# Kernel tuning notes

Hardware: AMD Instinct MI355X
Metric: run time of the kernel (lower is better)

## Reference

```python
import jax, jax.numpy as jnp
import numpy as np
from jax import lax

B, T, CD = 128, 4096, 2
HID, K = 64, 5
FIN = CD * 3 + 4  # 10 scorer input channels
PAD = K // 2
LEARNED_W = 0.5


def setup_inputs() -> dict:
    key = jax.random.key(0)
    ks = jax.random.split(key, 10)
    trajectory = jax.random.normal(ks[0], (B, T, CD), jnp.float32)
    intervals = jax.random.uniform(ks[1], (B, T), jnp.float32, 0.01, 1.0)
    lengths = jax.random.randint(ks[2], (B,), T // 2, T + 1)
    attention_mask = (jnp.arange(T)[None, :] < lengths[:, None]).astype(jnp.float32)
    observed_mask = (jax.random.uniform(ks[3], (B, T)) > 0.3).astype(jnp.float32)
    w1 = jax.random.normal(ks[4], (HID, FIN, K), jnp.float32) / np.sqrt(FIN * K)
    b1 = jnp.zeros((HID,), jnp.float32)
    w2 = jax.random.normal(ks[5], (HID, HID, K), jnp.float32) / np.sqrt(HID * K)
    b2 = jnp.zeros((HID,), jnp.float32)
    w3 = jax.random.normal(ks[6], (1, HID, 1), jnp.float32) / np.sqrt(HID)
    b3 = jnp.zeros((1,), jnp.float32)
    return dict(trajectory=trajectory, intervals=intervals, attention_mask=attention_mask,
                observed_mask=observed_mask, w1=w1, b1=b1, w2=w2, b2=b2, w3=w3, b3=b3)


def _conv1d(x, w, pad):  # x: [B,C,T], w: [O,I,K]
    return lax.conv_general_dilated(x, w, (1,), [(pad, pad)],
                                    dimension_numbers=('NCH', 'OIH', 'NCH'))


def _safe_norm(v):  # grad-safe L2 norm over last dim, exact forward
    s2 = jnp.sum(v * v, axis=-1)
    return jnp.where(s2 > 0, jnp.sqrt(jnp.where(s2 > 0, s2, 1.0)), 0.0)


def _robust_normalize(values, mask):
    # vectorized version of per-sample 95th-percentile scaling
    valid = mask > 0.5
    n = jnp.sum(valid, axis=1)  # [B] int
    s = jnp.sort(jnp.where(valid, values, jnp.inf), axis=1)  # valid ascending, inf last
    idx = jnp.maximum(1, jnp.ceil(n.astype(jnp.float32) * 0.95).astype(jnp.int32)) - 1
    idx = jnp.clip(idx, 0, T - 1)
    scale = jnp.abs(jnp.take_along_axis(s, idx[:, None], axis=1))[:, 0]
    maxabs = jnp.max(jnp.where(valid, jnp.abs(values), 0.0), axis=1)
    scale = jnp.where(scale < 1e-6, maxabs, scale)
    out = values / jnp.maximum(scale, 1e-6)[:, None]
    out = jnp.where((n > 0)[:, None], out, 0.0)
    return out * mask


def _smooth(scores, mask):  # avg_pool1d k=K stride 1 pad K//2 (count_include_pad=True)
    kern = jnp.full((1, 1, K), 1.0 / K, scores.dtype)
    sm = _conv1d(scores[:, None, :], kern, PAD)[:, 0]
    return sm * mask


def _forward(trajectory, intervals, attention_mask, observed_mask, w1, b1, w2, b2, w3, b3):
    mask = attention_mask
    vm = mask > 0.5
    pm = (vm[:, 1:] & vm[:, :-1]).astype(trajectory.dtype)  # [B,T-1]

    def mdiff3(x):
        d = (x[:, 1:] - x[:, :-1]) * pm[..., None]
        return jnp.concatenate([jnp.zeros_like(x[:, :1]), d], axis=1)

    def mdiff2(x):
        d = (x[:, 1:] - x[:, :-1]) * pm
        return jnp.concatenate([jnp.zeros_like(x[:, :1]), d], axis=1)

    mt = trajectory * mask[..., None]
    coord_diff = mdiff3(mt)
    delta_t = jnp.maximum(intervals[..., None], 1e-3)
    interval_feat = intervals * mask
    velocity = coord_diff / delta_t * mask[..., None]
    acceleration = mdiff3(velocity) / delta_t * mask[..., None]
    speed = _safe_norm(velocity) * mask
    speed_change = jnp.abs(mdiff2(speed)) * mask
    accel_norm = _safe_norm(acceleration) * mask
    heading = jnp.arctan2(velocity[..., 1], velocity[..., 0])
    rhc = heading[:, 1:] - heading[:, :-1]
    rhc = jnp.abs(jnp.arctan2(jnp.sin(rhc), jnp.cos(rhc)))
    heading_change = jnp.concatenate([jnp.zeros_like(speed[:, :1]), rhc * pm], axis=1) * mask
    obs_feat = observed_mask * mask
    ot = jnp.abs(observed_mask[:, 1:] - observed_mask[:, :-1]) * pm
    observed_transition = jnp.concatenate([jnp.zeros_like(speed[:, :1]), ot], axis=1) * mask

    feats = jnp.concatenate([mt, velocity, acceleration, speed[..., None],
                             heading_change[..., None], interval_feat[..., None],
                             obs_feat[..., None]], axis=-1) * mask[..., None]  # [B,T,10]

    # rule scores
    scores = (0.35 * _robust_normalize(heading_change, mask)
              + 0.30 * _robust_normalize(accel_norm, mask)
              + 0.25 * _robust_normalize(speed_change, mask)
              + 0.10 * jnp.clip(observed_transition, 0.0, 1.0) * mask)
    scores = _smooth(scores, mask)
    rule_scores = jnp.clip(_robust_normalize(scores, mask), 0.0, 1.0) * mask

    # learned scores (Conv1d stack, exact GELU like torch default)
    x = feats.transpose(0, 2, 1)  # [B,10,T]
    h = jax.nn.gelu(_conv1d(x, w1, PAD) + b1[None, :, None], approximate=False)
    h = jax.nn.gelu(_conv1d(h, w2, PAD) + b2[None, :, None], approximate=False)
    learned = jax.nn.sigmoid((_conv1d(h, w3, 0) + b3[None, :, None])[:, 0]) * mask
    learned = jnp.clip(_smooth(learned, mask), 0.0, 1.0)

    out = (1.0 - LEARNED_W) * rule_scores + LEARNED_W * learned
    return jnp.clip(out, 0.0, 1.0) * mask


def reference(trajectory, intervals, attention_mask, observed_mask, w1, b1, w2, b2, w3, b3):
    return _forward(trajectory, intervals, attention_mask, observed_mask, w1, b1, w2, b2, w3, b3)
```

## Files before the change

kernel.cpp:

```cpp
#include <hip/hip_runtime.h>

namespace {

constexpr int B_ = 128;
constexpr int T_ = 4096;
constexpr int BT = B_ * T_;
constexpr int CT = 64;
constexpr unsigned NOINS = 0xFFFFFFFFu;

constexpr size_t OFF_W1F = 0;
constexpr size_t OFF_W2F = 2048;
constexpr size_t OFF_F16 = 16384;
constexpr size_t OFF_HC  = OFF_F16 + (size_t)BT * 5;
constexpr size_t OFF_AN  = OFF_HC + (size_t)BT;
constexpr size_t OFF_SC  = OFF_AN + (size_t)BT;
constexpr size_t OFF_OT  = OFF_SC + (size_t)BT;
constexpr size_t OFF_LP  = OFF_OT + (size_t)BT;

typedef _Float16 half8 __attribute__((ext_vector_type(8)));
typedef _Float16 half4 __attribute__((ext_vector_type(4)));
typedef _Float16 half2_t __attribute__((ext_vector_type(2)));
typedef float f32x4 __attribute__((ext_vector_type(4)));

__device__ __forceinline__ float clip01(float x) { return fminf(fmaxf(x, 0.f), 1.f); }

__device__ __forceinline__ float gelu_tanh(float x) {
  float x2 = x * x;
  float q = x * __builtin_fmaf(-0.10294444f, x2, -2.3022077f);
  float e = __builtin_amdgcn_exp2f(q);
  return x * __builtin_amdgcn_rcpf(1.0f + e);
}

__device__ __forceinline__ void compute_feats(
    const float* __restrict__ tr, const float* __restrict__ iv,
    const float* __restrict__ mk, const float* __restrict__ om, int t,
    float* __restrict__ f , float* anv_out, float* scv_out, float* otv_out) {
  float m  = mk[t];
  float m1 = (t >= 1) ? mk[t - 1] : 0.f;
  float m2 = (t >= 2) ? mk[t - 2] : 0.f;
  float pm01 = (m > 0.5f && m1 > 0.5f) ? 1.f : 0.f;
  float pm12 = (m1 > 0.5f && m2 > 0.5f) ? 1.f : 0.f;
  float x0x = tr[2 * t] * m, x0y = tr[2 * t + 1] * m;
  float x1x = 0.f, x1y = 0.f, x2x = 0.f, x2y = 0.f;
  if (t >= 1) { x1x = tr[2 * (t - 1)] * m1; x1y = tr[2 * (t - 1) + 1] * m1; }
  if (t >= 2) { x2x = tr[2 * (t - 2)] * m2; x2y = tr[2 * (t - 2) + 1] * m2; }
  float dt0 = fmaxf(iv[t], 1e-3f);
  float dt1 = (t >= 1) ? fmaxf(iv[t - 1], 1e-3f) : 1e-3f;
  float vx = 0.f, vy = 0.f, v1x = 0.f, v1y = 0.f;
  if (t >= 1) { vx = (x0x - x1x) * pm01 / dt0 * m; vy = (x0y - x1y) * pm01 / dt0 * m; }
  if (t >= 2) { v1x = (x1x - x2x) * pm12 / dt1 * m1; v1y = (x1y - x2y) * pm12 / dt1 * m1; }
  float ax = 0.f, ay = 0.f;
  if (t >= 1) { ax = (vx - v1x) * pm01 / dt0 * m; ay = (vy - v1y) * pm01 / dt0 * m; }
  float s2 = vx * vx + vy * vy;
  float speed = (s2 > 0.f ? sqrtf(s2) : 0.f) * m;
  float s21 = v1x * v1x + v1y * v1y;
  float speed1 = (s21 > 0.f ? sqrtf(s21) : 0.f) * m1;
  float scv = (t >= 1) ? fabsf((speed - speed1) * pm01) * m : 0.f;
  float a2 = ax * ax + ay * ay;
  float anv = (a2 > 0.f ? sqrtf(a2) : 0.f) * m;
  float hcv = 0.f;
  if (t >= 1) {
    bool z0 = (vx == 0.f && vy == 0.f);
    bool z1 = (v1x == 0.f && v1y == 0.f);
    float yy, xx;
    if (z1)      { yy = vy;  xx = vx; }
    else if (z0) { yy = v1y; xx = v1x; }
    else { yy = vy * v1x - vx * v1y; xx = vx * v1x + vy * v1y; }
    hcv = fabsf(atan2f(yy, xx)) * pm01 * m;
  }
  float obs = om[t] * m;
  float otv = (t >= 1) ? fminf(fabsf(om[t] - om[t - 1]) * pm01 * m, 1.f) : 0.f;
  float itf = iv[t] * m;
  f[0] = x0x; f[1] = x0y; f[2] = vx; f[3] = vy; f[4] = ax; f[5] = ay;
  f[6] = speed; f[7] = hcv; f[8] = itf; f[9] = obs;
  *anv_out = anv; *scv_out = scv; *otv_out = otv;
}

__global__ __launch_bounds__(256)
void featurize_k(const float* __restrict__ traj, const float* __restrict__ intervals,
                 const float* __restrict__ amask, const float* __restrict__ omask,
                 const float* __restrict__ w1g, const float* __restrict__ w2g,
                 _Float16* __restrict__ feats16, float* __restrict__ hc,
                 float* __restrict__ an, float* __restrict__ sc, float* __restrict__ ot,
                 half8* __restrict__ w1f, half8* __restrict__ w2f) {
  int idx = blockIdx.x * 256 + threadIdx.x;
  int b = idx >> 12;
  int t = idx & (T_ - 1);
  float f[10], anv, scv, otv;
  compute_feats(traj + (size_t)b * T_ * 2, intervals + (size_t)b * T_,
                amask + (size_t)b * T_, omask + (size_t)b * T_, t, f, &anv, &scv, &otv);
  half2_t* fd = reinterpret_cast<half2_t*>(feats16) + (size_t)idx * 5;
#pragma unroll
  for (int q = 0; q < 5; ++q) {
    half2_t pk;
    pk[0] = (_Float16)(f[2 * q] * 0.015625f);
    pk[1] = (_Float16)(f[2 * q + 1] * 0.015625f);
    fd[q] = pk;
  }
  hc[idx] = f[7]; an[idx] = anv; sc[idx] = scv; ot[idx] = otv;

  if (blockIdx.x < 12) {
    int gid = blockIdx.x * 256 + threadIdx.x;
    if (gid < 48 * 64) {
      int fid = gid >> 6, lane = gid & 63;
      int qd = lane >> 4, ln = lane & 15;
      half8 v;
      if (fid < 8) {
        int m = fid >> 1, kk = fid & 1;
        int o = m * 16 + ln;
#pragma unroll
        for (int j = 0; j < 8; ++j) {
          int ck = kk * 32 + qd * 8 + j;
          float val = 0.f;
          if (ck < 50) { int k_ = ck / 10, c = ck - 10 * k_; val = w1g[o * 50 + c * 5 + k_]; }
          v[j] = (_Float16)val;
        }
        w1f[fid * 64 + lane] = v;
      } else {
        int f2 = fid - 8;
        int k = f2 >> 3, kk = (f2 >> 2) & 1, m = f2 & 3;
        int o = m * 16 + ln;
#pragma unroll
        for (int j = 0; j < 8; ++j) {
          int ic = kk * 32 + qd * 8 + j;
          v[j] = (_Float16)w2g[o * 320 + ic * 5 + k];
        }
        w2f[f2 * 64 + lane] = v;
      }
    }
  }
}

__global__ __launch_bounds__(256)
void conv_k(const _Float16* __restrict__ feats16, const half8* __restrict__ w1f,
            const float* __restrict__ b1g, const half8* __restrict__ w2f,
            const float* __restrict__ b2g, const float* __restrict__ w3g,
            const float* __restrict__ b3g, const float* __restrict__ amask,
            float* __restrict__ lp) {
  __shared__ _Float16 sIm[80 * 72];
  __shared__ _Float16 sH1[68 * 72];
  __shared__ float sPart[2][64];
  _Float16* sF16 = sH1;
  int tid = threadIdx.x;
  int lane = tid & 63, w = tid >> 6;
  int qd = lane >> 4, ln = lane & 15;
  int tile = blockIdx.x, b = blockIdx.y;
  int t0 = tile * CT;

  const unsigned* gfd = reinterpret_cast<const unsigned*>(feats16 + (size_t)b * T_ * 10);
  unsigned* sFd = reinterpret_cast<unsigned*>(sF16);
  int dbase = (t0 - 4) * 5;
  for (int s = tid; s < 360; s += 256) {
    int gi = dbase + s;
    sFd[s] = (gi >= 0 && gi < T_ * 5) ? gfd[gi] : 0u;
  }
  for (int s = tid; s < 560; s += 256) {
    int jt = s / 7, d = s - jt * 7;
    *reinterpret_cast<unsigned*>(&sIm[jt * 72 + 50 + 2 * d]) = 0u;
  }
  __syncthreads();
  unsigned* sId = reinterpret_cast<unsigned*>(sIm);
  for (int s = tid; s < 340; s += 256) {
    int jt = s / 5, k = s - jt * 5;
    const unsigned* src = sFd + (jt + k) * 5;
    unsigned* dst = sId + jt * 36 + k * 5;
#pragma unroll
    for (int q = 0; q < 5; ++q) dst[q] = src[q];
  }
  __syncthreads();

  {
    int m = w;
    half8 a1k0 = w1f[(m * 2 + 0) * 64 + lane];
    half8 a1k1 = w1f[(m * 2 + 1) * 64 + lane];
    f32x4 bv = *reinterpret_cast<const f32x4*>(&b1g[m * 16 + qd * 4]);
    f32x4 b1s;
#pragma unroll
    for (int r = 0; r < 4; ++r) b1s[r] = bv[r] * 0.015625f;
#pragma unroll
    for (int tl = 0; tl < 5; ++tl) {
      int jt = tl * 16 + ln;
      half8 bf0 = *reinterpret_cast<const half8*>(&sIm[jt * 72 + qd * 8]);
      half8 bf1 = *reinterpret_cast<const half8*>(&sIm[jt * 72 + 32 + qd * 8]);
      f32x4 acc = b1s;
      acc = __builtin_amdgcn_mfma_f32_16x16x32_f16(a1k0, bf0, acc, 0, 0, 0);
      acc = __builtin_amdgcn_mfma_f32_16x16x32_f16(a1k1, bf1, acc, 0, 0, 0);
      if (jt < 68) {
        int t = t0 - 2 + jt;
        bool inr = (t >= 0 && t < T_);
        half4 hv;
#pragma unroll
        for (int r = 0; r < 4; ++r) {
          float h = inr ? gelu_tanh(acc[r] * 64.f) * 0.0625f : 0.f;
          hv[r] = (_Float16)h;
        }
        *reinterpret_cast<half4*>(&sH1[jt * 72 + m * 16 + qd * 4]) = hv;
      }
    }
  }
  __syncthreads();

  int p = w & 1, nq = w >> 1;
  f32x4 acc2[2][2];
#pragma unroll
  for (int dm = 0; dm < 2; ++dm) {
    f32x4 bv = *reinterpret_cast<const f32x4*>(&b2g[(2 * p + dm) * 16 + qd * 4]);
#pragma unroll
    for (int dn = 0; dn < 2; ++dn)
#pragma unroll
      for (int r = 0; r < 4; ++r) acc2[dm][dn][r] = bv[r] * 0.0625f;
  }
#pragma unroll
  for (int k = 0; k < 5; ++k) {
#pragma unroll
    for (int kk = 0; kk < 2; ++kk) {
      half8 A0 = w2f[((k * 2 + kk) * 4 + 2 * p + 0) * 64 + lane];
      half8 A1 = w2f[((k * 2 + kk) * 4 + 2 * p + 1) * 64 + lane];
      half8 B0 = *reinterpret_cast<const half8*>(
          &sH1[((2 * nq + 0) * 16 + ln + k) * 72 + kk * 32 + qd * 8]);
      half8 B1 = *reinterpret_cast<const half8*>(
          &sH1[((2 * nq + 1) * 16 + ln + k) * 72 + kk * 32 + qd * 8]);
      acc2[0][0] = __builtin_amdgcn_mfma_f32_16x16x32_f16(A0, B0, acc2[0][0], 0, 0, 0);
      acc2[0][1] = __builtin_amdgcn_mfma_f32_16x16x32_f16(A0, B1, acc2[0][1], 0, 0, 0);
      acc2[1][0] = __builtin_amdgcn_mfma_f32_16x16x32_f16(A1, B0, acc2[1][0], 0, 0, 0);
      acc2[1][1] = __builtin_amdgcn_mfma_f32_16x16x32_f16(A1, B1, acc2[1][1], 0, 0, 0);
    }
  }
  f32x4 w3a = *reinterpret_cast<const f32x4*>(&w3g[(2 * p + 0) * 16 + qd * 4]);
  f32x4 w3b = *reinterpret_cast<const f32x4*>(&w3g[(2 * p + 1) * 16 + qd * 4]);
#pragma unroll
  for (int dn = 0; dn < 2; ++dn) {
    float s = 0.f;
#pragma unroll
    for (int r = 0; r < 4; ++r) s += w3a[r] * gelu_tanh(acc2[0][dn][r] * 16.f);
#pragma unroll
    for (int r = 0; r < 4; ++r) s += w3b[r] * gelu_tanh(acc2[1][dn][r] * 16.f);
    s += __shfl_xor(s, 16);
    s += __shfl_xor(s, 32);
    if (lane < 16) sPart[p][(2 * nq + dn) * 16 + lane] = s;
  }
  __syncthreads();
  if (tid < 64) {
    int t = t0 + tid;
    float logit = sPart[0][tid] + sPart[1][tid] + b3g[0];
    float m = amask[(size_t)b * T_ + t];
    float e = __builtin_amdgcn_exp2f(logit * -1.4426950408889634f);
    lp[(size_t)b * T_ + t] = m * __builtin_amdgcn_rcpf(1.f + e);
  }
}

__device__ __forceinline__ void scan4096(unsigned (*hist)[4096], int j, int tid, int lane,
                                         int wv, unsigned (*sW)[16], uint4& v,
                                         unsigned& ps, unsigned& incl) {
  v = *reinterpret_cast<uint4*>(&hist[j][tid * 4]);
  uint4 zz = {0u, 0u, 0u, 0u};
  *reinterpret_cast<uint4*>(&hist[j][tid * 4]) = zz;
  ps = v.x + v.y + v.z + v.w;
  incl = ps;
#pragma unroll
  for (int off = 1; off < 64; off <<= 1) {
    unsigned tv = __shfl_up(incl, off, 64);
    if (lane >= off) incl += tv;
  }
  if (lane == 63) sW[j][wv] = incl;
}
__device__ __forceinline__ void resolve4096(const unsigned (*sW)[16], int j, int tid, int wv,
                                            uint4 v, unsigned ps, unsigned incl, unsigned k,
                                            unsigned* selb, unsigned* selk) {
  unsigned woff = 0;
  for (int i = 0; i < wv; ++i) woff += sW[j][i];
  incl += woff;
  unsigned excl = incl - ps;
  if (excl <= k && k < incl) {
    unsigned vv[4] = {v.x, v.y, v.z, v.w};
    unsigned run = excl;
    int c = 0;
#pragma unroll
    for (; c < 3; ++c) {
      if (run + vv[c] > k) break;
      run += vv[c];
    }
    *selb = (unsigned)(tid * 4 + c);
    *selk = k - run;
  }
}
__device__ __forceinline__ void scan256(unsigned (*hist)[4096], int j, int tid, int lane,
                                        int wv, unsigned (*sW)[16], unsigned& v,
                                        unsigned& incl) {
  v = (tid < 256) ? hist[j][tid] : 0u;
  if (tid < 256) hist[j][tid] = 0u;
  incl = v;
#pragma unroll
  for (int off = 1; off < 64; off <<= 1) {
    unsigned tv = __shfl_up(incl, off, 64);
    if (lane >= off) incl += tv;
  }
  if (lane == 63) sW[j][wv] = incl;
}
__device__ __forceinline__ void resolve256(const unsigned (*sW)[16], int j, int tid, int wv,
                                           unsigned v, unsigned incl, unsigned k,
                                           unsigned* selb) {
  unsigned woff = 0;
  for (int i = 0; i < wv; ++i) woff += sW[j][i];
  incl += woff;
  unsigned excl = incl - v;
  if (excl <= k && k < incl) *selb = (unsigned)tid;
}

__global__ __launch_bounds__(1024)
void ruleselect_k(const float* __restrict__ hc, const float* __restrict__ an,
                  const float* __restrict__ sc, const float* __restrict__ ot,
                  const float* __restrict__ amask, const float* __restrict__ lp,
                  float* __restrict__ out) {
  __shared__ unsigned hist3[3][4096];
  __shared__ float vbuf[4096];
  __shared__ unsigned selB[2][4];
  __shared__ unsigned selK[2][4];
  __shared__ unsigned sW3[3][16];
  __shared__ float sM3[3][16];
  __shared__ int iCnt[16];
  int b = blockIdx.x, tid = threadIdx.x;
  int lane = tid & 63, wv = tid >> 6;
  const float* mk = amask + (size_t)b * T_;
  const float* h0 = hc + (size_t)b * T_;
  const float* a0 = an + (size_t)b * T_;
  const float* s0 = sc + (size_t)b * T_;
  const float* o0 = ot + (size_t)b * T_;

  float mv0[4], mv1[4], mv2[4], otv[4], mreg[4];
  int cnt = 0;
#pragma unroll
  for (int r = 0; r < 4; ++r) {
    int t = tid + 1024 * r;
    mv0[r] = h0[t]; mv1[r] = a0[t]; mv2[r] = s0[t]; otv[r] = o0[t];
    mreg[r] = mk[t];
    cnt += (mreg[r] > 0.5f);
  }
#pragma unroll
  for (int off = 32; off; off >>= 1) cnt += __shfl_xor(cnt, off);
  if (lane == 0) iCnt[wv] = cnt;
  {
    unsigned* hflat = &hist3[0][0];
    for (int i = tid; i < 3 * 4096; i += 1024) hflat[i] = 0u;
  }
  unsigned u0[4], u1[4], u2[4];
  float mxa = 0.f, mxb = 0.f, mxc = 0.f;
#pragma unroll
  for (int r = 0; r < 4; ++r) {
    bool valid = mreg[r] > 0.5f;
    unsigned b0 = __float_as_uint(mv0[r]); if ((int)b0 < 0) b0 = 0u;
    unsigned b1 = __float_as_uint(mv1[r]); if ((int)b1 < 0) b1 = 0u;
    unsigned b2 = __float_as_uint(mv2[r]); if ((int)b2 < 0) b2 = 0u;
    u0[r] = valid ? b0 : NOINS;
    u1[r] = valid ? b1 : NOINS;
    u2[r] = valid ? b2 : NOINS;
    if (valid) {
      mxa = fmaxf(mxa, fabsf(mv0[r]));
      mxb = fmaxf(mxb, fabsf(mv1[r]));
      mxc = fmaxf(mxc, fabsf(mv2[r]));
    }
  }
#pragma unroll
  for (int off = 32; off; off >>= 1) {
    mxa = fmaxf(mxa, __shfl_xor(mxa, off));
    mxb = fmaxf(mxb, __shfl_xor(mxb, off));
    mxc = fmaxf(mxc, __shfl_xor(mxc, off));
  }
  if (lane == 0) { sM3[0][wv] = mxa; sM3[1][wv] = mxb; sM3[2][wv] = mxc; }
  __syncthreads();
  int n = 0;
#pragma unroll
  for (int i = 0; i < 16; ++i) n += iCnt[i];
  int cidx = (int)ceilf((float)n * 0.95f);
  if (cidx < 1) cidx = 1;
  unsigned kidx = (unsigned)(cidx - 1);
  if (kidx > (unsigned)(T_ - 1)) kidx = T_ - 1;
  float mx3a = sM3[0][0], mx3b = sM3[1][0], mx3c = sM3[2][0];
#pragma unroll
  for (int i = 1; i < 16; ++i) {
    mx3a = fmaxf(mx3a, sM3[0][i]);
    mx3b = fmaxf(mx3b, sM3[1][i]);
    mx3c = fmaxf(mx3c, sM3[2][i]);
  }

#pragma unroll
  for (int r = 0; r < 4; ++r) {
    if (u0[r] != NOINS) atomicAdd(&hist3[0][u0[r] >> 20], 1u);
    if (u1[r] != NOINS) atomicAdd(&hist3[1][u1[r] >> 20], 1u);
    if (u2[r] != NOINS) atomicAdd(&hist3[2][u2[r] >> 20], 1u);
  }
  __syncthreads();
  uint4 v40, v41, v42; unsigned ps0, ps1, ps2, in0, in1, in2;
  scan4096(hist3, 0, tid, lane, wv, sW3, v40, ps0, in0);
  scan4096(hist3, 1, tid, lane, wv, sW3, v41, ps1, in1);
  scan4096(hist3, 2, tid, lane, wv, sW3, v42, ps2, in2);
  __syncthreads();
  resolve4096(sW3, 0, tid, wv, v40, ps0, in0, kidx, &selB[1][0], &selK[1][0]);
  resolve4096(sW3, 1, tid, wv, v41, ps1, in1, kidx, &selB[1][1], &selK[1][1]);
  resolve4096(sW3, 2, tid, wv, v42, ps2, in2, kidx, &selB[1][2], &selK[1][2]);
  __syncthreads();
  unsigned p1_0 = selB[1][0], p1_1 = selB[1][1], p1_2 = selB[1][2];
  unsigned k2_0 = selK[1][0], k2_1 = selK[1][1], k2_2 = selK[1][2];
#pragma unroll
  for (int r = 0; r < 4; ++r) {
    if (u0[r] != NOINS && (u0[r] >> 20) == p1_0) atomicAdd(&hist3[0][(u0[r] >> 8) & 0xFFFu], 1u);
    if (u1[r] != NOINS && (u1[r] >> 20) == p1_1) atomicAdd(&hist3[1][(u1[r] >> 8) & 0xFFFu], 1u);
    if (u2[r] != NOINS && (u2[r] >> 20) == p1_2) atomicAdd(&hist3[2][(u2[r] >> 8) & 0xFFFu], 1u);
  }
  __syncthreads();
  scan4096(hist3, 0, tid, lane, wv, sW3, v40, ps0, in0);
  scan4096(hist3, 1, tid, lane, wv, sW3, v41, ps1, in1);
  scan4096(hist3, 2, tid, lane, wv, sW3, v42, ps2, in2);
  __syncthreads();
  resolve4096(sW3, 0, tid, wv, v40, ps0, in0, k2_0, &selB[0][0], &selK[0][0]);
  resolve4096(sW3, 1, tid, wv, v41, ps1, in1, k2_1, &selB[0][1], &selK[0][1]);
  resolve4096(sW3, 2, tid, wv, v42, ps2, in2, k2_2, &selB[0][2], &selK[0][2]);
  __syncthreads();
  unsigned p2_0 = selB[0][0], p2_1 = selB[0][1], p2_2 = selB[0][2];
  unsigned k3_0 = selK[0][0], k3_1 = selK[0][1], k3_2 = selK[0][2];
  unsigned pf0 = (p1_0 << 12) | p2_0, pf1 = (p1_1 << 12) | p2_1, pf2 = (p1_2 << 12) | p2_2;
#pragma unroll
  for (int r = 0; r < 4; ++r) {
    if (u0[r] != NOINS && (u0[r] >> 8) == pf0) atomicAdd(&hist3[0][u0[r] & 0xFFu], 1u);
    if (u1[r] != NOINS && (u1[r] >> 8) == pf1) atomicAdd(&hist3[1][u1[r] & 0xFFu], 1u);
    if (u2[r] != NOINS && (u2[r] >> 8) == pf2) atomicAdd(&hist3[2][u2[r] & 0xFFu], 1u);
  }
  __syncthreads();
  unsigned s80, s81, s82;
  scan256(hist3, 0, tid, lane, wv, sW3, s80, in0);
  scan256(hist3, 1, tid, lane, wv, sW3, s81, in1);
  scan256(hist3, 2, tid, lane, wv, sW3, s82, in2);
  __syncthreads();
  resolve256(sW3, 0, tid, wv, s80, in0, k3_0, &selB[1][0]);
  resolve256(sW3, 1, tid, wv, s81, in1, k3_1, &selB[1][1]);
  resolve256(sW3, 2, tid, wv, s82, in2, k3_2, &selB[1][2]);
  __syncthreads();
  float kth0 = fabsf(__uint_as_float((p1_0 << 20) | (p2_0 << 8) | selB[1][0]));
  float kth1 = fabsf(__uint_as_float((p1_1 << 20) | (p2_1 << 8) | selB[1][1]));
  float kth2 = fabsf(__uint_as_float((p1_2 << 20) | (p2_2 << 8) | selB[1][2]));
  float sc0 = fmaxf((kth0 < 1e-6f) ? mx3a : kth0, 1e-6f);
  float sc1 = fmaxf((kth1 < 1e-6f) ? mx3b : kth1, 1e-6f);
  float sc2 = fmaxf((kth2 < 1e-6f) ? mx3c : kth2, 1e-6f);

#pragma unroll
  for (int r = 0; r < 4; ++r) {
    int t = tid + 1024 * r;
    float v = 0.f;
    if (n > 0) {
      v = 0.35f * (mv0[r] / sc0) + 0.30f * (mv1[r] / sc1)
        + 0.25f * (mv2[r] / sc2) + 0.10f * otv[r];
    }
    vbuf[t] = v;
  }
  __syncthreads();
  float sm[4];
#pragma unroll
  for (int r = 0; r < 4; ++r) {
    int t = tid + 1024 * r;
    float s = 0.f;
#pragma unroll
    for (int d = -2; d <= 2; ++d) {
      int tt = t + d;
      if (tt >= 0 && tt < T_) s += vbuf[tt];
    }
    sm[r] = s * 0.2f * mreg[r];
  }
  unsigned uu[4];
  float mxs = 0.f;
#pragma unroll
  for (int r = 0; r < 4; ++r) {
    bool valid = mreg[r] > 0.5f;
    unsigned ub = __float_as_uint(sm[r]); if ((int)ub < 0) ub = 0u;
    uu[r] = valid ? ub : NOINS;
    if (valid) mxs = fmaxf(mxs, fabsf(sm[r]));
  }
#pragma unroll
  for (int off = 32; off; off >>= 1) mxs = fmaxf(mxs, __shfl_xor(mxs, off));
  if (lane == 0) sM3[0][wv] = mxs;
#pragma unroll
  for (int r = 0; r < 4; ++r)
    if (uu[r] != NOINS) atomicAdd(&hist3[0][uu[r] >> 20], 1u);
  __syncthreads();
  const float* lprow = lp + (size_t)b * T_;
#pragma unroll
  for (int r = 0; r < 4; ++r) {
    int t = tid + 1024 * r;
    vbuf[t] = lprow[t];
  }
  float mx4 = sM3[0][0];
#pragma unroll
  for (int i = 1; i < 16; ++i) mx4 = fmaxf(mx4, sM3[0][i]);
  scan4096(hist3, 0, tid, lane, wv, sW3, v40, ps0, in0);
  __syncthreads();
  resolve4096(sW3, 0, tid, wv, v40, ps0, in0, kidx, &selB[1][3], &selK[1][3]);
  __syncthreads();
  unsigned q1 = selB[1][3], kq2 = selK[1][3];
#pragma unroll
  for (int r = 0; r < 4; ++r)
    if (uu[r] != NOINS && (uu[r] >> 20) == q1) atomicAdd(&hist3[0][(uu[r] >> 8) & 0xFFFu], 1u);
  __syncthreads();
  scan4096(hist3, 0, tid, lane, wv, sW3, v40, ps0, in0);
  __syncthreads();
  resolve4096(sW3, 0, tid, wv, v40, ps0, in0, kq2, &selB[0][3], &selK[0][3]);
  __syncthreads();
  unsigned q2 = selB[0][3], kq3 = selK[0][3];
  unsigned qf = (q1 << 12) | q2;
#pragma unroll
  for (int r = 0; r < 4; ++r)
    if (uu[r] != NOINS && (uu[r] >> 8) == qf) atomicAdd(&hist3[0][uu[r] & 0xFFu], 1u);
  __syncthreads();
  scan256(hist3, 0, tid, lane, wv, sW3, s80, in0);
  __syncthreads();
  resolve256(sW3, 0, tid, wv, s80, in0, kq3, &selB[1][3]);
  __syncthreads();
  float kth4 = fabsf(__uint_as_float((q1 << 20) | (q2 << 8) | selB[1][3]));
  float scale4 = fmaxf((kth4 < 1e-6f) ? mx4 : kth4, 1e-6f);
  float* orow = out + (size_t)b * T_;
#pragma unroll
  for (int r = 0; r < 4; ++r) {
    int t = tid + 1024 * r;
    float rv = (n > 0) ? sm[r] / scale4 : 0.f;
    rv = clip01(rv) * mreg[r];
    float ssum = 0.f;
#pragma unroll
    for (int d = -2; d <= 2; ++d) {
      int tt = t + d;
      if (tt >= 0 && tt < T_) ssum += vbuf[tt];
    }
    float learned = clip01(ssum * 0.2f * mreg[r]);
    orow[t] = clip01(0.5f * rv + 0.5f * learned) * mreg[r];
  }
}

}

extern "C" void kernel_launch(void* const* d_in, const int* in_sizes, int n_in,
                              void* d_out, int out_size, void* d_ws, size_t ws_size,
                              hipStream_t stream) {
  const float* traj      = (const float*)d_in[0];
  const float* intervals = (const float*)d_in[1];
  const float* amask     = (const float*)d_in[2];
  const float* omask     = (const float*)d_in[3];
  const float* w1        = (const float*)d_in[4];
  const float* b1        = (const float*)d_in[5];
  const float* w2        = (const float*)d_in[6];
  const float* b2        = (const float*)d_in[7];
  const float* w3        = (const float*)d_in[8];
  const float* b3        = (const float*)d_in[9];
  float* out = (float*)d_out;
  float* ws = (float*)d_ws;

  _Float16* feats16 = (_Float16*)(ws + OFF_F16);
  float* hc = ws + OFF_HC;
  float* an = ws + OFF_AN;
  float* sc = ws + OFF_SC;
  float* ot = ws + OFF_OT;
  float* lp = ws + OFF_LP;
  half8* w1f = (half8*)(ws + OFF_W1F);
  half8* w2f = (half8*)(ws + OFF_W2F);

  featurize_k<<<BT / 256, 256, 0, stream>>>(traj, intervals, amask, omask, w1, w2,
                                            feats16, hc, an, sc, ot, w1f, w2f);
  conv_k<<<dim3(T_ / CT, B_), 256, 0, stream>>>(feats16, w1f, b1, w2f, b2, w3, b3,
                                                amask, lp);
  ruleselect_k<<<B_, 1024, 0, stream>>>(hc, an, sc, ot, amask, lp, out);
}
```

Measured before the change: 150.6 us.

## Pack rule metrics into float4, use fast atan2/reciprocal, set conv occupancy hint

Interleaves the four per-timestep rule metrics into one float4 array, so featurize writes and ruleselect reads them with single vector accesses instead of four separate streams. Replaces the divisions by dt with one Newton-refined reciprocal and replaces atan2f with a polynomial minimax approximation of |atan2|. Adds a min-blocks-per-CU launch bound of 7 to the conv kernel to push register allocation toward higher occupancy. The atan approximation and reciprocal change the heading-change values slightly, and the occupancy hint may cause register spills in conv_k.

```diff
diff --git a/kernel.cpp b/kernel.cpp
--- a/kernel.cpp
+++ b/kernel.cpp
@@ -11,11 +11,8 @@
 constexpr size_t OFF_W1F = 0;
 constexpr size_t OFF_W2F = 2048;
 constexpr size_t OFF_F16 = 16384;
-constexpr size_t OFF_HC  = OFF_F16 + (size_t)BT * 5;
-constexpr size_t OFF_AN  = OFF_HC + (size_t)BT;
-constexpr size_t OFF_SC  = OFF_AN + (size_t)BT;
-constexpr size_t OFF_OT  = OFF_SC + (size_t)BT;
-constexpr size_t OFF_LP  = OFF_OT + (size_t)BT;
+constexpr size_t OFF_MET = OFF_F16 + (size_t)BT * 5;
+constexpr size_t OFF_LP  = OFF_MET + (size_t)BT * 4;
 
 typedef _Float16 half8 __attribute__((ext_vector_type(8)));
 typedef _Float16 half4 __attribute__((ext_vector_type(4)));
@@ -29,6 +26,28 @@
   float q = x * __builtin_fmaf(-0.10294444f, x2, -2.3022077f);
   float e = __builtin_amdgcn_exp2f(q);
   return x * __builtin_amdgcn_rcpf(1.0f + e);
+}
+
+__device__ __forceinline__ float rcp_nr(float d) {
+  float r = __builtin_amdgcn_rcpf(d);
+  return r * __builtin_fmaf(-d, r, 2.0f);
+}
+
+__device__ __forceinline__ float fabs_atan2_fast(float y, float x) {
+  float ay = fabsf(y), ax = fabsf(x);
+  float mn = fminf(ax, ay), mx = fmaxf(ax, ay);
+  float rc = rcp_nr(mx);
+  float r = (mx > 0.f) ? mn * rc : 0.f;
+  float s = r * r;
+  float p = __builtin_fmaf(s, -0.01172120f, 0.05265332f);
+  p = __builtin_fmaf(s, p, -0.11643287f);
+  p = __builtin_fmaf(s, p, 0.19354346f);
+  p = __builtin_fmaf(s, p, -0.33262347f);
+  p = __builtin_fmaf(s, p, 0.99997726f);
+  float t = r * p;
+  if (ay > ax) t = 1.5707963267948966f - t;
+  if (x < 0.f) t = 3.141592653589793f - t;
+  return t;
 }
 
 __device__ __forceinline__ void compute_feats(
@@ -46,11 +65,13 @@
   if (t >= 2) { x2x = tr[2 * (t - 2)] * m2; x2y = tr[2 * (t - 2) + 1] * m2; }
   float dt0 = fmaxf(iv[t], 1e-3f);
   float dt1 = (t >= 1) ? fmaxf(iv[t - 1], 1e-3f) : 1e-3f;
+  float inv0 = rcp_nr(dt0);
+  float inv1 = rcp_nr(dt1);
   float vx = 0.f, vy = 0.f, v1x = 0.f, v1y = 0.f;
-  if (t >= 1) { vx = (x0x - x1x) * pm01 / dt0 * m; vy = (x0y - x1y) * pm01 / dt0 * m; }
-  if (t >= 2) { v1x = (x1x - x2x) * pm12 / dt1 * m1; v1y = (x1y - x2y) * pm12 / dt1 * m1; }
+  if (t >= 1) { vx = (x0x - x1x) * pm01 * inv0 * m; vy = (x0y - x1y) * pm01 * inv0 * m; }
+  if (t >= 2) { v1x = (x1x - x2x) * pm12 * inv1 * m1; v1y = (x1y - x2y) * pm12 * inv1 * m1; }
   float ax = 0.f, ay = 0.f;
-  if (t >= 1) { ax = (vx - v1x) * pm01 / dt0 * m; ay = (vy - v1y) * pm01 / dt0 * m; }
+  if (t >= 1) { ax = (vx - v1x) * pm01 * inv0 * m; ay = (vy - v1y) * pm01 * inv0 * m; }
   float s2 = vx * vx + vy * vy;
   float speed = (s2 > 0.f ? sqrtf(s2) : 0.f) * m;
   float s21 = v1x * v1x + v1y * v1y;
@@ -66,7 +87,7 @@
     if (z1)      { yy = vy;  xx = vx; }
     else if (z0) { yy = v1y; xx = v1x; }
     else { yy = vy * v1x - vx * v1y; xx = vx * v1x + vy * v1y; }
-    hcv = fabsf(atan2f(yy, xx)) * pm01 * m;
+    hcv = fabs_atan2_fast(yy, xx) * pm01 * m;
   }
   float obs = om[t] * m;
   float otv = (t >= 1) ? fminf(fabsf(om[t] - om[t - 1]) * pm01 * m, 1.f) : 0.f;
@@ -80,8 +101,7 @@
 void featurize_k(const float* __restrict__ traj, const float* __restrict__ intervals,
                  const float* __restrict__ amask, const float* __restrict__ omask,
                  const float* __restrict__ w1g, const float* __restrict__ w2g,
-                 _Float16* __restrict__ feats16, float* __restrict__ hc,
-                 float* __restrict__ an, float* __restrict__ sc, float* __restrict__ ot,
+                 _Float16* __restrict__ feats16, float4* __restrict__ met,
                  half8* __restrict__ w1f, half8* __restrict__ w2f) {
   int idx = blockIdx.x * 256 + threadIdx.x;
   int b = idx >> 12;
@@ -97,7 +117,7 @@
     pk[1] = (_Float16)(f[2 * q + 1] * 0.015625f);
     fd[q] = pk;
   }
-  hc[idx] = f[7]; an[idx] = anv; sc[idx] = scv; ot[idx] = otv;
+  met[idx] = make_float4(f[7], anv, scv, otv);
 
   if (blockIdx.x < 12) {
     int gid = blockIdx.x * 256 + threadIdx.x;
@@ -131,7 +151,7 @@
   }
 }
 
-__global__ __launch_bounds__(256)
+__global__ __launch_bounds__(256, 7)
 void conv_k(const _Float16* __restrict__ feats16, const half8* __restrict__ w1f,
             const float* __restrict__ b1g, const half8* __restrict__ w2f,
             const float* __restrict__ b2g, const float* __restrict__ w3g,
@@ -308,10 +328,8 @@
 }
 
 __global__ __launch_bounds__(1024)
-void ruleselect_k(const float* __restrict__ hc, const float* __restrict__ an,
-                  const float* __restrict__ sc, const float* __restrict__ ot,
-                  const float* __restrict__ amask, const float* __restrict__ lp,
-                  float* __restrict__ out) {
+void ruleselect_k(const float4* __restrict__ met, const float* __restrict__ amask,
+                  const float* __restrict__ lp, float* __restrict__ out) {
   __shared__ unsigned hist3[3][4096];
   __shared__ float vbuf[4096];
   __shared__ unsigned selB[2][4];
@@ -322,17 +340,15 @@
   int b = blockIdx.x, tid = threadIdx.x;
   int lane = tid & 63, wv = tid >> 6;
   const float* mk = amask + (size_t)b * T_;
-  const float* h0 = hc + (size_t)b * T_;
-  const float* a0 = an + (size_t)b * T_;
-  const float* s0 = sc + (size_t)b * T_;
-  const float* o0 = ot + (size_t)b * T_;
+  const float4* mrow = met + (size_t)b * T_;
 
   float mv0[4], mv1[4], mv2[4], otv[4], mreg[4];
   int cnt = 0;
 #pragma unroll
   for (int r = 0; r < 4; ++r) {
     int t = tid + 1024 * r;
-    mv0[r] = h0[t]; mv1[r] = a0[t]; mv2[r] = s0[t]; otv[r] = o0[t];
+    float4 v = mrow[t];
+    mv0[r] = v.x; mv1[r] = v.y; mv2[r] = v.z; otv[r] = v.w;
     mreg[r] = mk[t];
     cnt += (mreg[r] > 0.5f);
   }
@@ -551,17 +567,14 @@
   float* ws = (float*)d_ws;
 
   _Float16* feats16 = (_Float16*)(ws + OFF_F16);
-  float* hc = ws + OFF_HC;
-  float* an = ws + OFF_AN;
-  float* sc = ws + OFF_SC;
-  float* ot = ws + OFF_OT;
+  float4* met = (float4*)(ws + OFF_MET);
   float* lp = ws + OFF_LP;
   half8* w1f = (half8*)(ws + OFF_W1F);
   half8* w2f = (half8*)(ws + OFF_W2F);
 
   featurize_k<<<BT / 256, 256, 0, stream>>>(traj, intervals, amask, omask, w1, w2,
-                                            feats16, hc, an, sc, ot, w1f, w2f);
+                                            feats16, met, w1f, w2f);
   conv_k<<<dim3(T_ / CT, B_), 256, 0, stream>>>(feats16, w1f, b1, w2f, b2, w3, b3,
                                                 amask, lp);
-  ruleselect_k<<<B_, 1024, 0, stream>>>(hc, an, sc, ot, amask, lp, out);
-}
+  ruleselect_k<<<B_, 1024, 0, stream>>>(met, amask, lp, out);
+}
```

Result: faster. 147.6 us (-2.0%).
